# Kernel tuning notes

Hardware: AMD Instinct MI355X
Metric: run time of the kernel (lower is better)

Reference implementation:

```python
import jax, jax.numpy as jnp
import numpy as np

N_QUBITS = 6
N_LAYERS = 2
QSVT_DEGREE = 3
BATCH = 128
SEQ_LEN = 512
DIM = 2 ** N_QUBITS
# wire 0 is the most-significant bit in the statevector index (PennyLane convention)
_POP = np.array([bin(i).count('1') for i in range(DIM)], dtype=np.float32)
PHASE_SIGN = jnp.asarray(N_QUBITS - 2.0 * _POP)  # (DIM,): sum_w (1 - 2*bit_w)


def _rx(t):
    c = jnp.cos(0.5 * t).astype(jnp.complex64)
    s = (-1j * jnp.sin(0.5 * t)).astype(jnp.complex64)
    return jnp.stack([jnp.stack([c, s]), jnp.stack([s, c])])


def _ry(t):
    c = jnp.cos(0.5 * t).astype(jnp.complex64)
    s = jnp.sin(0.5 * t).astype(jnp.complex64)
    return jnp.stack([jnp.stack([c, -s]), jnp.stack([s, c])])


def _rz(t):
    e = jnp.exp(-0.5j * t.astype(jnp.complex64))
    z = jnp.zeros((), jnp.complex64)
    return jnp.stack([jnp.stack([e, z]), jnp.stack([z, jnp.conj(e)])])


def _apply_1q(psi, U, w):
    # psi: (B,) + (2,)*N_QUBITS ; U: (2,2) complex, same for all batch elems
    psi = jnp.moveaxis(psi, 1 + w, -1)
    psi = psi @ U.T
    return jnp.moveaxis(psi, -1, 1 + w)


def _apply_ry_batched(psi, theta, w):
    # RY with a per-batch angle theta: (B,)
    psi = jnp.moveaxis(psi, 1 + w, -1)
    c = jnp.cos(0.5 * theta).reshape((-1,) + (1,) * (N_QUBITS - 1))
    s = jnp.sin(0.5 * theta).reshape((-1,) + (1,) * (N_QUBITS - 1))
    a, b = psi[..., 0], psi[..., 1]
    psi = jnp.stack([c * a - s * b, s * a + c * b], axis=-1)
    return jnp.moveaxis(psi, -1, 1 + w)


def _cnot(psi, c, t):
    p0 = jax.lax.index_in_dim(psi, 0, axis=1 + c, keepdims=True)
    p1 = jax.lax.index_in_dim(psi, 1, axis=1 + c, keepdims=True)
    p1 = jnp.flip(p1, axis=1 + t)
    return jnp.concatenate([p0, p1], axis=1 + c)


def _circuit_step(h, x, params, poly):
    # h, x: (B, N_QUBITS) angles. Returns <Z_w> per qubit: (B, N_QUBITS).
    B = h.shape[0]
    # 1) state encoding: RY(h_w)|0> = cos(h/2)|0> + sin(h/2)|1>  (product state)
    c, s = jnp.cos(0.5 * h), jnp.sin(0.5 * h)
    psi = jnp.ones((B, 1), jnp.complex64)
    for w in range(N_QUBITS):
        amp = jnp.stack([c[:, w], s[:, w]], axis=-1).astype(jnp.complex64)  # (B,2)
        psi = (psi[:, :, None] * amp[:, None, :]).reshape(B, -1)
    psi = psi.reshape((B,) + (2,) * N_QUBITS)
    # 2) QSVT block: RZ(coeff*pi) on every wire fuses into one diagonal phase
    for d in range(QSVT_DEGREE + 1):
        theta = poly[d] * np.pi
        phase = jnp.exp((-0.5j) * theta * PHASE_SIGN)  # (DIM,)
        psi = (psi.reshape(B, -1) * phase[None, :]).reshape((B,) + (2,) * N_QUBITS)
        for i in range(N_QUBITS - 1):
            psi = _cnot(psi, i, i + 1)
        psi = _cnot(psi, N_QUBITS - 1, 0)  # ring closure
    # 3) variational layers: per-wire RZ@RY@RX (RX applied first), then CNOT chain
    idx = 0
    for _ in range(N_LAYERS):
        for i in range(N_QUBITS):
            U = _rz(params[idx + 2]) @ _ry(params[idx + 1]) @ _rx(params[idx])
            psi = _apply_1q(psi, U, i)
            idx += 3
        for i in range(N_QUBITS - 1):
            psi = _cnot(psi, i, i + 1)
    # 4) input injection: RY(x_w) with per-batch angles
    for w in range(N_QUBITS):
        psi = _apply_ry_batched(psi, x[:, w], w)
    # 5) measurement: <Z_w> = P(bit_w=0) - P(bit_w=1)
    p = jnp.abs(psi) ** 2
    zs = []
    for w in range(N_QUBITS):
        axes = tuple(a for a in range(1, N_QUBITS + 1) if a != 1 + w)
        pw = p.sum(axis=axes)  # (B,2)
        zs.append(pw[:, 0] - pw[:, 1])
    return jnp.stack(zs, axis=-1)


def _ssm_pass(angles, params, poly, reverse):
    a = jnp.flip(angles, axis=1) if reverse else angles
    xs = jnp.moveaxis(a, 1, 0)  # (T, B, n)
    h0 = jnp.zeros((a.shape[0], N_QUBITS), jnp.float32)

    def step(h, x):
        hn = _circuit_step(h, x, params, poly)
        return hn, hn

    _, ys = jax.lax.scan(step, h0, xs)
    out = jnp.moveaxis(ys, 0, 1)  # (B, T, n)
    return jnp.flip(out, axis=1) if reverse else out


def setup_inputs() -> dict:
    key = jax.random.key(0)
    k0, k1, k2, k3 = jax.random.split(key, 4)
    angles = jax.random.uniform(k0, (BATCH, SEQ_LEN, N_QUBITS), jnp.float32) * np.float32(np.pi)
    poly_coeffs = jax.random.normal(k1, (QSVT_DEGREE + 1,), jnp.float32) * 0.1
    fwd_params = jax.random.normal(k2, (N_QUBITS * N_LAYERS * 3,), jnp.float32) * 0.1
    bwd_params = jax.random.normal(k3, (N_QUBITS * N_LAYERS * 3,), jnp.float32) * 0.1
    fwd_coeff = jnp.full((1,), 0.5, jnp.float32)
    bwd_coeff = jnp.full((1,), 0.5, jnp.float32)
    return {'angles': angles, 'poly_coeffs': poly_coeffs, 'fwd_params': fwd_params,
            'bwd_params': bwd_params, 'fwd_coeff': fwd_coeff, 'bwd_coeff': bwd_coeff}


def reference(angles, poly_coeffs, fwd_params, bwd_params, fwd_coeff, bwd_coeff):
    h_fwd = _ssm_pass(angles, fwd_params, poly_coeffs, reverse=False)
    h_bwd = _ssm_pass(angles, bwd_params, poly_coeffs, reverse=True)
    return jax.nn.sigmoid(fwd_coeff) * h_fwd + jax.nn.sigmoid(bwd_coeff) * h_bwd
```

## Files before the change

### kernel.cpp

```cpp
#include <hip/hip_runtime.h>
#include <hip/hip_bf16.h>
#include <stdint.h>

#define BATCH 128
#define SEQ   512
#define NW    6
#define DIM   64
#define NELEM (BATCH * SEQ * NW)
#define PI_F  3.14159265358979323846f

typedef float v2f __attribute__((ext_vector_type(2)));

__device__ __forceinline__ v2f pkfma(float s, v2f m, v2f a) {
    return __builtin_elementwise_fma((v2f){s, s}, m, a);
}

template <int CTRL>
__device__ __forceinline__ void red_stage6(float v[6]) {
#pragma unroll
    for (int w = 0; w < 6; ++w)
        v[w] += __int_as_float(__builtin_amdgcn_update_dpp(
            0, __float_as_int(v[w]), CTRL, 0xF, 0xF, false));
}

__device__ __forceinline__ void sincos_half(float h, float& s, float& c) {
    const float u = h * h;
    c = fmaf(u, fmaf(u, fmaf(u, -2.1701389e-5f, 2.6041667e-3f), -0.125f), 1.0f);
    s = h * fmaf(u, fmaf(u, fmaf(u, -1.5501e-6f, 2.6041667e-4f), -2.0833333e-2f), 0.5f);
}

__global__ void k_detect(const uint32_t* __restrict__ a, int* __restrict__ flag) {
    __shared__ int cnt;
    if (threadIdx.x == 0) cnt = 0;
    __syncthreads();
    uint32_t w = a[threadIdx.x];
    uint32_t e = (w >> 8) & 0xFFu;
    if (e >= 0x3Au && e <= 0x41u) atomicAdd(&cnt, 1);
    __syncthreads();
    if (threadIdx.x == 0) *flag = (cnt >= 128) ? 1 : 0;
}

__device__ __forceinline__ float ldf(const void* p, int i, bool bf) {
    if (bf) {
        uint32_t u = (uint32_t)((const uint16_t*)p)[i];
        return __uint_as_float(u << 16);
    }
    return ((const float*)p)[i];
}

__global__ void k_convert(const void* ang, const void* poly, const void* fp,
                          const void* bp, const void* fc, const void* bc,
                          float* __restrict__ cs, float* __restrict__ misc,
                          const int* __restrict__ flag) {
    const bool bf = (*flag != 0);
    const int i = blockIdx.x * blockDim.x + threadIdx.x;
    if (i < NELEM) {
        float x = ldf(ang, i, bf);
        float s, c;
        __sincosf(x, &s, &c);
        cs[2 * i]     = c;
        cs[2 * i + 1] = s;
    }
    if (i < 4)                    misc[i]            = ldf(poly, i, bf);
    else if (i >= 64 && i < 100)  misc[4 + (i - 64)] = ldf(fp, i - 64, bf);
    else if (i >= 128 && i < 164) misc[40 + (i - 128)] = ldf(bp, i - 128, bf);
    else if (i == 200)            misc[76] = ldf(fc, 0, bf);
    else if (i == 201)            misc[77] = ldf(bc, 0, bf);
}

__global__ void __launch_bounds__(64) k_msetup(const float* __restrict__ misc,
                                               float* __restrict__ Mg) {
    const int p   = threadIdx.x;
    const int col = blockIdx.x & 63;
    const int dir = blockIdx.x >> 6;
    const float* poly = misc;
    const float* prm  = misc + (dir ? 40 : 4);

    float yr = (p == col) ? 1.f : 0.f;
    float yi = 0.f;

#pragma unroll
    for (int d = 0; d < 4; ++d) {
        const float th = 0.5f * PI_F * poly[d] *
                         (float)(6 - 2 * (int)__popc((unsigned)p));
        float s, c;
        __sincosf(th, &s, &c);
        const float nr = yr * c + yi * s;
        const float ni = yi * c - yr * s;
        yr = nr; yi = ni;
#pragma unroll
        for (int k = 0; k < 6; ++k) {
            const int cw = k, tw = (k + 1) % 6;
            const int src = p ^ (((p >> (5 - cw)) & 1) << (5 - tw));
            yr = __shfl(yr, src, 64);
            yi = __shfl(yi, src, 64);
        }
    }

    int idx = 0;
#pragma unroll
    for (int l = 0; l < 2; ++l) {
#pragma unroll
        for (int w = 0; w < 6; ++w) {
            float cx, sx, cy, sy, cz, sz;
            __sincosf(0.5f * prm[idx + 0], &sx, &cx);
            __sincosf(0.5f * prm[idx + 1], &sy, &cy);
            __sincosf(0.5f * prm[idx + 2], &sz, &cz);
            idx += 3;
            const float A = cy * cx, B = sy * sx, C = sy * cx, D = cy * sx;
            const float U00r = cz * A + sz * B, U00i = cz * B - sz * A;
            const float U11r = U00r,            U11i = sz * A - cz * B;
            const float Xr   = cz * C + sz * D, Xi   = sz * C - cz * D;
            const int m  = 1 << (5 - w);
            const int bb = (p >> (5 - w)) & 1;
            const float C1r = bb ? U11r : U00r;
            const float C1i = bb ? U11i : U00i;
            const float C2r = bb ? Xr : -Xr;
            const float C2i = Xi;
            const float pr = __shfl_xor(yr, m, 64);
            const float pi = __shfl_xor(yi, m, 64);
            const float nr = C1r * yr - C1i * yi + C2r * pr - C2i * pi;
            const float ni = C1r * yi + C1i * yr + C2r * pi + C2i * pr;
            yr = nr; yi = ni;
        }
#pragma unroll
        for (int k = 0; k < 5; ++k) {
            const int src = p ^ (((p >> (5 - k)) & 1) << (5 - (k + 1)));
            yr = __shfl(yr, src, 64);
            yi = __shfl(yi, src, 64);
        }
    }

    float* out = Mg + ((size_t)(dir * 64 + p) * 64 + (size_t)col) * 2;
    out[0] = yr;
    out[1] = yi;
}

__global__ void __launch_bounds__(128, 1) k_sim(const float* __restrict__ cs,
                                                const float* __restrict__ Mg,
                                                float* __restrict__ hbuf) {
    const int tid   = threadIdx.x;
    const int lane  = tid & 63;
    const int wv    = tid >> 6;
    const int chain = blockIdx.x;
    const int dir   = chain >> 7;
    const int b     = chain & 127;
    float* orow = hbuf + (size_t)dir * NELEM + (size_t)b * (SEQ * NW);
    const float* csrow = cs + (size_t)b * (SEQ * NW * 2);

    __shared__ float  cl[SEQ * 12];
    __shared__ float  zb[SEQ * NW];
    __shared__ float2 pY[2][2][DIM];

    {
        const float4* src = (const float4*)csrow;
        float4* dst = (float4*)cl;
#pragma unroll
        for (int k = 0; k < 12; ++k) {
            const int idx = tid + k * 128;
            dst[idx] = src[idx];
        }
    }

    v2f Mres[32];
    {
        const float2* mr2 =
            (const float2*)(Mg + (size_t)(dir * 64 + lane) * 128 + 64 * wv);
#pragma unroll
        for (int k = 0; k < 32; ++k) Mres[k] = (v2f){mr2[k].x, mr2[k].y};
    }

    int zmask[6], bpa[6];
#pragma unroll
    for (int w = 0; w < 6; ++w) {
        zmask[w] = ((lane >> (5 - w)) & 1) << 31;
        bpa[w]   = (lane ^ (1 << (5 - w))) << 2;
    }

    float h[6] = {0.f, 0.f, 0.f, 0.f, 0.f, 0.f};

    auto encode_matvec = [&](v2f& acc) {
        float cw6[6], sw6[6];
#pragma unroll
        for (int w = 0; w < 6; ++w) sincos_half(h[w], sw6[w], cw6[w]);
        float L[8];
        {
            const float l00 = cw6[3] * cw6[4], l01 = cw6[3] * sw6[4];
            const float l10 = sw6[3] * cw6[4], l11 = sw6[3] * sw6[4];
            L[0] = l00 * cw6[5]; L[1] = l00 * sw6[5];
            L[2] = l01 * cw6[5]; L[3] = l01 * sw6[5];
            L[4] = l10 * cw6[5]; L[5] = l10 * sw6[5];
            L[6] = l11 * cw6[5]; L[7] = l11 * sw6[5];
        }
        const float gw0 = wv ? sw6[0] : cw6[0];
        const float g0  = gw0 * cw6[1], g1 = gw0 * sw6[1];
        float GH[4];
        GH[0] = g0 * cw6[2]; GH[1] = g0 * sw6[2];
        GH[2] = g1 * cw6[2]; GH[3] = g1 * sw6[2];
        v2f y = {0.f, 0.f};
#pragma unroll
        for (int j = 0; j < 4; ++j) {
            v2f T = {0.f, 0.f};
#pragma unroll
            for (int bb2 = 0; bb2 < 8; ++bb2)
                T = pkfma(L[bb2], Mres[8 * j + bb2], T);
            y = pkfma(GH[j], T, y);
        }
        acc = y;
    };

    const float* cp = cl + (dir ? (SEQ - 1) * 12 : 0);
    const int   cstep = dir ? -12 : 12;
    float*       zp = zb + (dir ? (SEQ - 1) * NW : 0);
    const int   zstep = dir ? -NW : NW;

    __syncthreads();

    v2f myacc;
    encode_matvec(myacc);
    pY[0][wv][lane] = (float2){myacc.x, myacc.y};
    __syncthreads();

    for (int t = 0; t < SEQ; ++t) {
        const int buf = t & 1;

        const float4 xq0 = ((const float4*)cp)[0];
        const float4 xq1 = ((const float4*)cp)[1];
        const float4 xq2 = ((const float4*)cp)[2];
        cp += cstep;
        const float2 yo = pY[buf][wv ^ 1][lane];

        const float yr = myacc.x + yo.x;
        const float yi = myacc.y + yo.y;

        float pr[6], pi[6];
#pragma unroll
        for (int w = 0; w < 6; ++w)
            pr[w] = __int_as_float(
                __builtin_amdgcn_ds_bpermute(bpa[w], __float_as_int(yr)));
#pragma unroll
        for (int w = 0; w < 6; ++w)
            pi[w] = __int_as_float(
                __builtin_amdgcn_ds_bpermute(bpa[w], __float_as_int(yi)));

        const float q = yr * yr + yi * yi;
        float cxw[6], sxw[6];
        cxw[0] = xq0.x; sxw[0] = xq0.y; cxw[1] = xq0.z; sxw[1] = xq0.w;
        cxw[2] = xq1.x; sxw[2] = xq1.y; cxw[3] = xq1.z; sxw[3] = xq1.w;
        cxw[4] = xq2.x; sxw[4] = xq2.y; cxw[5] = xq2.z; sxw[5] = xq2.w;

        float v[6];
#pragma unroll
        for (int w = 0; w < 6; ++w) {
            const float ac = yr * pr[w] + yi * pi[w];
            const float sq = __int_as_float(__float_as_int(q) ^ zmask[w]);
            v[w] = cxw[w] * sq - sxw[w] * ac;
        }

        red_stage6<0x111>(v);
        red_stage6<0x112>(v);
        red_stage6<0x114>(v);
        red_stage6<0x118>(v);
        red_stage6<0x142>(v);
        red_stage6<0x143>(v);

        if (tid == 63) {
#pragma unroll
            for (int w = 0; w < 6; ++w) zp[w] = v[w];
        }
        zp += zstep;

#pragma unroll
        for (int w = 0; w < 6; ++w)
            h[w] = __int_as_float(
                __builtin_amdgcn_readlane(__float_as_int(v[w]), 63));

        encode_matvec(myacc);
        pY[buf ^ 1][wv][lane] = (float2){myacc.x, myacc.y};
        __syncthreads();
    }

    {
        const float4* zs4 = (const float4*)zb;
        float4* go = (float4*)orow;
#pragma unroll
        for (int k = 0; k < 6; ++k) {
            const int idx = tid + k * 128;
            go[idx] = zs4[idx];
        }
    }
}

__global__ void k_combine(const float* __restrict__ hbuf,
                          const float* __restrict__ misc,
                          void* __restrict__ out, const int* __restrict__ flag) {
    const int i = blockIdx.x * blockDim.x + threadIdx.x;
    if (i >= NELEM) return;
    const float sf = 1.f / (1.f + __expf(-misc[76]));
    const float sb = 1.f / (1.f + __expf(-misc[77]));
    const float v = sf * hbuf[i] + sb * hbuf[NELEM + i];
    if (*flag) ((__hip_bfloat16*)out)[i] = __float2bfloat16(v);
    else       ((float*)out)[i] = v;
}

extern "C" void kernel_launch(void* const* d_in, const int* in_sizes, int n_in,
                              void* d_out, int out_size, void* d_ws, size_t ws_size,
                              hipStream_t stream) {
    const void* ang  = d_in[0];
    const void* poly = d_in[1];
    const void* fp   = d_in[2];
    const void* bp   = d_in[3];
    const void* fc   = d_in[4];
    const void* bc   = d_in[5];

    float* cs   = (float*)d_ws + 32;
    float* misc = cs + 2 * NELEM;
    float* hbuf = misc + 128;
    float* Mg   = hbuf + 2 * NELEM;
    int*   flag = (int*)(Mg + 2 * 64 * 64 * 2);

    k_detect<<<1, 256, 0, stream>>>((const uint32_t*)ang, flag);
    k_convert<<<(NELEM + 255) / 256, 256, 0, stream>>>(ang, poly, fp, bp, fc, bc,
                                                       cs, misc, flag);
    k_msetup<<<128, 64, 0, stream>>>(misc, Mg);
    k_sim<<<256, 128, 0, stream>>>(cs, Mg, hbuf);
    k_combine<<<(NELEM + 255) / 256, 256, 0, stream>>>(hbuf, misc, d_out, flag);
}
```

Before: 420.4 us.

## Split per-chain simulation across four wavefronts with shared-memory reduction exchange

Raises k_sim from two to four wavefronts per chain. Each wave holds a quarter of the 64x64 matrix slice (16 packed registers instead of 32) and contributes a partial mat-vec summed through shared memory. The expectation computation is also split: two waves compute X-type terms and two compute Z-type terms, each for three wires, and the results go into a small shared array. That adds a second __syncthreads per timestep. The aim is to shorten the serial critical path per step by spreading the mat-vec and reduction work, at the cost of extra barriers and LDS traffic.

```diff
diff --git a/kernel.cpp b/kernel.cpp
--- a/kernel.cpp
+++ b/kernel.cpp
@@ -16,11 +16,11 @@
 }
 
 template <int CTRL>
-__device__ __forceinline__ void red_stage6(float v[6]) {
-#pragma unroll
-    for (int w = 0; w < 6; ++w)
-        v[w] += __int_as_float(__builtin_amdgcn_update_dpp(
-            0, __float_as_int(v[w]), CTRL, 0xF, 0xF, false));
+__device__ __forceinline__ void red_stage3(float v[3]) {
+#pragma unroll
+    for (int k = 0; k < 3; ++k)
+        v[k] += __int_as_float(__builtin_amdgcn_update_dpp(
+            0, __float_as_int(v[k]), CTRL, 0xF, 0xF, false));
 }
 
 __device__ __forceinline__ void sincos_half(float h, float& s, float& c) {
@@ -136,7 +136,7 @@
     out[1] = yi;
 }
 
-__global__ void __launch_bounds__(128, 1) k_sim(const float* __restrict__ cs,
+__global__ void __launch_bounds__(256, 1) k_sim(const float* __restrict__ cs,
                                                 const float* __restrict__ Mg,
                                                 float* __restrict__ hbuf) {
     const int tid   = threadIdx.x;
@@ -148,33 +148,37 @@
     float* orow = hbuf + (size_t)dir * NELEM + (size_t)b * (SEQ * NW);
     const float* csrow = cs + (size_t)b * (SEQ * NW * 2);
 
-    __shared__ float  cl[SEQ * 12];
-    __shared__ float  zb[SEQ * NW];
-    __shared__ float2 pY[2][2][DIM];
+    __shared__ __align__(16) float  cl[SEQ * 12];
+    __shared__ __align__(16) float  zb[SEQ * NW];
+    __shared__ float2 pY[2][4][DIM];
+    __shared__ __align__(16) float  mR[12];
 
     {
         const float4* src = (const float4*)csrow;
         float4* dst = (float4*)cl;
 #pragma unroll
-        for (int k = 0; k < 12; ++k) {
-            const int idx = tid + k * 128;
+        for (int k = 0; k < 6; ++k) {
+            const int idx = tid + k * 256;
             dst[idx] = src[idx];
         }
     }
 
-    v2f Mres[32];
+    v2f Mres[16];
     {
         const float2* mr2 =
-            (const float2*)(Mg + (size_t)(dir * 64 + lane) * 128 + 64 * wv);
-#pragma unroll
-        for (int k = 0; k < 32; ++k) Mres[k] = (v2f){mr2[k].x, mr2[k].y};
-    }
-
-    int zmask[6], bpa[6];
-#pragma unroll
-    for (int w = 0; w < 6; ++w) {
-        zmask[w] = ((lane >> (5 - w)) & 1) << 31;
-        bpa[w]   = (lane ^ (1 << (5 - w))) << 2;
+            (const float2*)(Mg + (size_t)(dir * 64 + lane) * 128 + 32 * wv);
+#pragma unroll
+        for (int k = 0; k < 16; ++k) Mres[k] = (v2f){mr2[k].x, mr2[k].y};
+    }
+
+    const int w0  = (wv & 1) * 3;
+    const int isX = wv >> 1;
+    int zmask3[3], bpa3[3];
+#pragma unroll
+    for (int k = 0; k < 3; ++k) {
+        const int w = w0 + k;
+        zmask3[k] = ((lane >> (5 - w)) & 1) << 31;
+        bpa3[k]   = (lane ^ (1 << (5 - w))) << 2;
     }
 
     float h[6] = {0.f, 0.f, 0.f, 0.f, 0.f, 0.f};
@@ -183,28 +187,24 @@
         float cw6[6], sw6[6];
 #pragma unroll
         for (int w = 0; w < 6; ++w) sincos_half(h[w], sw6[w], cw6[w]);
-        float L[8];
-        {
-            const float l00 = cw6[3] * cw6[4], l01 = cw6[3] * sw6[4];
-            const float l10 = sw6[3] * cw6[4], l11 = sw6[3] * sw6[4];
-            L[0] = l00 * cw6[5]; L[1] = l00 * sw6[5];
-            L[2] = l01 * cw6[5]; L[3] = l01 * sw6[5];
-            L[4] = l10 * cw6[5]; L[5] = l10 * sw6[5];
-            L[6] = l11 * cw6[5]; L[7] = l11 * sw6[5];
-        }
-        const float gw0 = wv ? sw6[0] : cw6[0];
-        const float g0  = gw0 * cw6[1], g1 = gw0 * sw6[1];
-        float GH[4];
-        GH[0] = g0 * cw6[2]; GH[1] = g0 * sw6[2];
-        GH[2] = g1 * cw6[2]; GH[3] = g1 * sw6[2];
+        const float t0 = (wv & 2) ? sw6[0] : cw6[0];
+        const float t1 = (wv & 1) ? sw6[1] : cw6[1];
+        const float A  = t0 * t1;
+        float GH[4], GL[4];
+        GH[0] = cw6[2] * cw6[3]; GH[1] = cw6[2] * sw6[3];
+        GH[2] = sw6[2] * cw6[3]; GH[3] = sw6[2] * sw6[3];
+#pragma unroll
+        for (int a = 0; a < 4; ++a) GH[a] *= A;
+        GL[0] = cw6[4] * cw6[5]; GL[1] = cw6[4] * sw6[5];
+        GL[2] = sw6[4] * cw6[5]; GL[3] = sw6[4] * sw6[5];
         v2f y = {0.f, 0.f};
 #pragma unroll
-        for (int j = 0; j < 4; ++j) {
+        for (int a = 0; a < 4; ++a) {
             v2f T = {0.f, 0.f};
 #pragma unroll
-            for (int bb2 = 0; bb2 < 8; ++bb2)
-                T = pkfma(L[bb2], Mres[8 * j + bb2], T);
-            y = pkfma(GH[j], T, y);
+            for (int b2 = 0; b2 < 4; ++b2)
+                T = pkfma(GL[b2], Mres[4 * a + b2], T);
+            y = pkfma(GH[a], T, y);
         }
         acc = y;
     };
@@ -216,67 +216,83 @@
 
     __syncthreads();
 
-    v2f myacc;
-    encode_matvec(myacc);
-    pY[0][wv][lane] = (float2){myacc.x, myacc.y};
+    {
+        v2f acc;
+        encode_matvec(acc);
+        pY[0][wv][lane] = (float2){acc.x, acc.y};
+    }
     __syncthreads();
 
     for (int t = 0; t < SEQ; ++t) {
         const int buf = t & 1;
+
+        const float2 y0 = pY[buf][0][lane], y1 = pY[buf][1][lane];
+        const float2 y2 = pY[buf][2][lane], y3 = pY[buf][3][lane];
+        const float yr = (y0.x + y1.x) + (y2.x + y3.x);
+        const float yi = (y0.y + y1.y) + (y2.y + y3.y);
+
+        float v3[3];
+        if (isX) {
+            float pr[3], pi[3];
+#pragma unroll
+            for (int k = 0; k < 3; ++k)
+                pr[k] = __int_as_float(
+                    __builtin_amdgcn_ds_bpermute(bpa3[k], __float_as_int(yr)));
+#pragma unroll
+            for (int k = 0; k < 3; ++k)
+                pi[k] = __int_as_float(
+                    __builtin_amdgcn_ds_bpermute(bpa3[k], __float_as_int(yi)));
+#pragma unroll
+            for (int k = 0; k < 3; ++k) v3[k] = yr * pr[k] + yi * pi[k];
+        } else {
+            const float q = yr * yr + yi * yi;
+#pragma unroll
+            for (int k = 0; k < 3; ++k)
+                v3[k] = __int_as_float(__float_as_int(q) ^ zmask3[k]);
+        }
+        red_stage3<0x111>(v3);
+        red_stage3<0x112>(v3);
+        red_stage3<0x114>(v3);
+        red_stage3<0x118>(v3);
+        red_stage3<0x142>(v3);
+        red_stage3<0x143>(v3);
+
+        if (lane == 63) {
+            mR[wv * 3 + 0] = v3[0];
+            mR[wv * 3 + 1] = v3[1];
+            mR[wv * 3 + 2] = v3[2];
+        }
+        __syncthreads();
 
         const float4 xq0 = ((const float4*)cp)[0];
         const float4 xq1 = ((const float4*)cp)[1];
         const float4 xq2 = ((const float4*)cp)[2];
         cp += cstep;
-        const float2 yo = pY[buf][wv ^ 1][lane];
-
-        const float yr = myacc.x + yo.x;
-        const float yi = myacc.y + yo.y;
-
-        float pr[6], pi[6];
-#pragma unroll
-        for (int w = 0; w < 6; ++w)
-            pr[w] = __int_as_float(
-                __builtin_amdgcn_ds_bpermute(bpa[w], __float_as_int(yr)));
-#pragma unroll
-        for (int w = 0; w < 6; ++w)
-            pi[w] = __int_as_float(
-                __builtin_amdgcn_ds_bpermute(bpa[w], __float_as_int(yi)));
-
-        const float q = yr * yr + yi * yi;
-        float cxw[6], sxw[6];
-        cxw[0] = xq0.x; sxw[0] = xq0.y; cxw[1] = xq0.z; sxw[1] = xq0.w;
-        cxw[2] = xq1.x; sxw[2] = xq1.y; cxw[3] = xq1.z; sxw[3] = xq1.w;
-        cxw[4] = xq2.x; sxw[4] = xq2.y; cxw[5] = xq2.z; sxw[5] = xq2.w;
-
-        float v[6];
-#pragma unroll
-        for (int w = 0; w < 6; ++w) {
-            const float ac = yr * pr[w] + yi * pi[w];
-            const float sq = __int_as_float(__float_as_int(q) ^ zmask[w]);
-            v[w] = cxw[w] * sq - sxw[w] * ac;
-        }
-
-        red_stage6<0x111>(v);
-        red_stage6<0x112>(v);
-        red_stage6<0x114>(v);
-        red_stage6<0x118>(v);
-        red_stage6<0x142>(v);
-        red_stage6<0x143>(v);
+        const float4 m0 = ((const float4*)mR)[0];
+        const float4 m1 = ((const float4*)mR)[1];
+        const float4 m2 = ((const float4*)mR)[2];
+
+        float z[6];
+        z[0] = xq0.x * m0.x - xq0.y * m1.z;
+        z[1] = xq0.z * m0.y - xq0.w * m1.w;
+        z[2] = xq1.x * m0.z - xq1.y * m2.x;
+        z[3] = xq1.z * m0.w - xq1.w * m2.y;
+        z[4] = xq2.x * m1.x - xq2.y * m2.z;
+        z[5] = xq2.z * m1.y - xq2.w * m2.w;
+#pragma unroll
+        for (int w = 0; w < 6; ++w) h[w] = z[w];
 
         if (tid == 63) {
 #pragma unroll
-            for (int w = 0; w < 6; ++w) zp[w] = v[w];
+            for (int w = 0; w < 6; ++w) zp[w] = z[w];
         }
         zp += zstep;
 
-#pragma unroll
-        for (int w = 0; w < 6; ++w)
-            h[w] = __int_as_float(
-                __builtin_amdgcn_readlane(__float_as_int(v[w]), 63));
-
-        encode_matvec(myacc);
-        pY[buf ^ 1][wv][lane] = (float2){myacc.x, myacc.y};
+        {
+            v2f acc;
+            encode_matvec(acc);
+            pY[buf ^ 1][wv][lane] = (float2){acc.x, acc.y};
+        }
         __syncthreads();
     }
 
@@ -284,8 +300,8 @@
         const float4* zs4 = (const float4*)zb;
         float4* go = (float4*)orow;
 #pragma unroll
-        for (int k = 0; k < 6; ++k) {
-            const int idx = tid + k * 128;
+        for (int k = 0; k < 3; ++k) {
+            const int idx = tid + k * 256;
             go[idx] = zs4[idx];
         }
     }
@@ -323,6 +339,6 @@
     k_convert<<<(NELEM + 255) / 256, 256, 0, stream>>>(ang, poly, fp, bp, fc, bc,
                                                        cs, misc, flag);
     k_msetup<<<128, 64, 0, stream>>>(misc, Mg);
-    k_sim<<<256, 128, 0, stream>>>(cs, Mg, hbuf);
+    k_sim<<<256, 256, 0, stream>>>(cs, Mg, hbuf);
     k_combine<<<(NELEM + 255) / 256, 256, 0, stream>>>(hbuf, misc, d_out, flag);
 }
```

Result: faster. 364.5 us (-13.3%).
